# Performance work log

Measured on AMD Instinct MI355X. Metric: run time of the kernel, lower is better.

Reference implementation:

```python
import jax, jax.numpy as jnp
import numpy as np

K = 172   # remainder Hadamard order (had172)
LOG2M = 6 # 2^6 = 64, so hadamard_dim = 172 * 64 = 11008


def _walsh_hadamard_matrix():
    # Dense form of the 6-stage FHT butterfly (Sylvester construction).
    H = np.array([[1.0]], dtype=np.float32)
    for _ in range(LOG2M):
        H = np.block([[H, H], [H, -H]])
    return jnp.asarray(H)  # [64, 64]


def setup_inputs() -> dict:
    key = jax.random.key(0)
    k1, k2 = jax.random.split(key)
    x = jax.random.normal(k1, (2, 4096, 11008), dtype=jnp.float32)
    had_rem_dim = jax.random.normal(k2, (K, K), dtype=jnp.float32) / np.float32(np.sqrt(K))
    return {"x": x, "had_rem_dim": had_rem_dim}


def reference(x, had_rem_dim):
    n = x.shape[-1]                      # 11008 = K * M
    M = n // K                           # 64
    scale = np.float32(1.0 / np.sqrt(n))
    H = _walsh_hadamard_matrix()         # [M, M]
    # view as (..., K, M): FHT over the power-of-two dim, scaled by 1/sqrt(n)
    xr = x.reshape(x.shape[:-1] + (K, M))
    y = jnp.einsum('...km,nm->...kn', xr, H) * scale
    # remainder Hadamard on the K dim: hadK @ input
    y = jnp.einsum('jk,...km->...jm', had_rem_dim, y)
    return y.reshape(x.shape)
```

## Files before the change

kernel.cpp:

```cpp
#include <hip/hip_runtime.h>
#include <hip/hip_bf16.h>

#define KREM 172
#define NDIM 11008
#define JPAD 176
#define KP_HAD 192
#define KP_Y 256

typedef __bf16 bf16x8 __attribute__((ext_vector_type(8)));
typedef float  f32x4  __attribute__((ext_vector_type(4)));
typedef float  f32x2  __attribute__((ext_vector_type(2)));

__global__ void prep_had_kernel(const float* __restrict__ had,
                                __bf16* __restrict__ hadB) {
  int idx = blockIdx.x * 256 + threadIdx.x;
  if (idx >= JPAD * KP_HAD) return;
  int j = idx / KP_HAD;
  int k = idx - j * KP_HAD;
  float v = (j < KREM && k < KREM) ? had[j * KREM + k] * 9.53115434e-3f : 0.0f;
  hadB[idx] = (__bf16)v;
}

__global__ void __launch_bounds__(256, 4) had_fused_kernel(
    const float* __restrict__ x, const __bf16* __restrict__ hadB,
    float* __restrict__ out) {
  __shared__ __bf16 Yt[64 * KP_Y];

  const int tid  = threadIdx.x;
  const int wave = tid >> 6;
  const int lane = tid & 63;
  const size_t rowoff = (size_t)blockIdx.x * NDIM;
  const float* xr   = x + rowoff;
  float*       outr = out + rowoff;

  if (tid < 64) {
    const int e = tid >> 3;
    __bf16* row = Yt + tid * KP_Y;
    const f32x4 z4 = {0.f, 0.f, 0.f, 0.f};
    *(f32x4*)(row + (((22 ^ e) << 3)))     = z4;
    *(f32x4*)(row + (((23 ^ e) << 3)))     = z4;
    *(f32x2*)(row + (((21 ^ e) << 3)) + 4) = (f32x2){0.f, 0.f};
  }

  const int grp = tid >> 3;
  const int lid = tid & 7;

#pragma unroll
  for (int p = 0; p < 6; ++p) {
    const int k = p * 32 + grp;
    if (k < KREM) {
      const float4* seg = (const float4*)(xr + k * 64 + lid * 8);
      float4 a = seg[0], b = seg[1];
      float v[8] = {a.x, a.y, a.z, a.w, b.x, b.y, b.z, b.w};
#pragma unroll
      for (int s = 1; s <= 4; s <<= 1) {
#pragma unroll
        for (int i = 0; i < 8; ++i) {
          if ((i & s) == 0) {
            float u0 = v[i], u1 = v[i + s];
            v[i] = u0 + u1;
            v[i + s] = u0 - u1;
          }
        }
      }
#pragma unroll
      for (int s = 1; s <= 4; s <<= 1) {
        const float sgn = (lid & s) ? -1.0f : 1.0f;
#pragma unroll
        for (int i = 0; i < 8; ++i) {
          float t = __shfl_xor(v[i], s, 64);
          v[i] = __builtin_fmaf(v[i], sgn, t);
        }
      }
      const int kb = k >> 3, ko = k & 7;
      const int kbs = (kb ^ lid) << 3;
#pragma unroll
      for (int i = 0; i < 8; ++i) {
        Yt[(lid * 8 + i) * KP_Y + kbs + ko] = (__bf16)v[i];
      }
    }
  }
  __syncthreads();

  const int l15 = lane & 15;
  const int q   = lane >> 4;
  const int njt = (wave < 3) ? 3 : 2;

#pragma unroll 1
  for (int jl = 0; jl < njt; ++jl) {
    const int jt   = wave + jl * 4;
    const int jrow = jt * 16 + l15;
    const __bf16* hb = hadB + jrow * KP_HAD;
    f32x4 acc[4] = {};
    __builtin_amdgcn_s_setprio(1);
#pragma unroll
    for (int kc = 0; kc < 6; ++kc) {
      const int kbase = kc * 32 + q * 8;
      const bf16x8 bfr = *(const bf16x8*)&hb[kbase];
#pragma unroll
      for (int nt = 0; nt < 4; ++nt) {
        const int n  = nt * 16 + l15;
        const int kb = (kbase >> 3) ^ (n >> 3);
        const bf16x8 afr = *(const bf16x8*)&Yt[n * KP_Y + (kb << 3)];
        acc[nt] = __builtin_amdgcn_mfma_f32_16x16x32_bf16(afr, bfr, acc[nt],
                                                          0, 0, 0);
      }
    }
    __builtin_amdgcn_s_setprio(0);
    if (jrow < KREM) {
#pragma unroll
      for (int nt = 0; nt < 4; ++nt) {
        *(f32x4*)(outr + jrow * 64 + nt * 16 + q * 4) = acc[nt];
      }
    }
  }
}

extern "C" void kernel_launch(void* const* d_in, const int* in_sizes, int n_in,
                              void* d_out, int out_size, void* d_ws, size_t ws_size,
                              hipStream_t stream) {
  const float* x   = (const float*)d_in[0];
  const float* had = (const float*)d_in[1];
  __bf16* hadB = (__bf16*)d_ws;
  float* out = (float*)d_out;
  const int rows = in_sizes[0] / NDIM;

  hipLaunchKernelGGL(prep_had_kernel, dim3((JPAD * KP_HAD + 255) / 256),
                     dim3(256), 0, stream, had, hadB);
  hipLaunchKernelGGL(had_fused_kernel, dim3(rows), dim3(256), 0, stream,
                     x, hadB, out);
}
```

Baseline: 617.6 us.

## Reorder MFMA loop to reuse LDS fragments across j-tiles and use DPP shuffles

The GEMM phase is restructured so the k-chunk loop is outermost. Each wave loads its four Yt A-fragments from LDS once per chunk and reuses them for all of its j-tiles, with 3x4 accumulators held live. This cuts LDS reads about threefold but raises VGPR pressure, which may hurt occupancy under the 4-block launch bound. The xor-1 and xor-2 butterfly shuffles are also replaced with DPP quad_perm moves instead of ds_bpermute-based __shfl_xor.

```diff
diff --git a/kernel.cpp b/kernel.cpp
--- a/kernel.cpp
+++ b/kernel.cpp
@@ -19,6 +19,14 @@
   int k = idx - j * KP_HAD;
   float v = (j < KREM && k < KREM) ? had[j * KREM + k] * 9.53115434e-3f : 0.0f;
   hadB[idx] = (__bf16)v;
+}
+
+__device__ __forceinline__ float dpp_xor(float x, const int ctrl_is_b1) {
+  int s = __builtin_bit_cast(int, x);
+  int t = ctrl_is_b1
+              ? __builtin_amdgcn_update_dpp(0, s, 0xB1, 0xF, 0xF, true)
+              : __builtin_amdgcn_update_dpp(0, s, 0x4E, 0xF, 0xF, true);
+  return __builtin_bit_cast(float, t);
 }
 
 __global__ void __launch_bounds__(256, 4) had_fused_kernel(
@@ -45,6 +53,10 @@
   const int grp = tid >> 3;
   const int lid = tid & 7;
 
+  const float sgn1 = (lid & 1) ? -1.0f : 1.0f;
+  const float sgn2 = (lid & 2) ? -1.0f : 1.0f;
+  const float sgn4 = (lid & 4) ? -1.0f : 1.0f;
+
 #pragma unroll
   for (int p = 0; p < 6; ++p) {
     const int k = p * 32 + grp;
@@ -64,13 +76,19 @@
         }
       }
 #pragma unroll
-      for (int s = 1; s <= 4; s <<= 1) {
-        const float sgn = (lid & s) ? -1.0f : 1.0f;
+      for (int i = 0; i < 8; ++i) {
+        float t = dpp_xor(v[i], 1);
+        v[i] = __builtin_fmaf(v[i], sgn1, t);
+      }
 #pragma unroll
-        for (int i = 0; i < 8; ++i) {
-          float t = __shfl_xor(v[i], s, 64);
-          v[i] = __builtin_fmaf(v[i], sgn, t);
-        }
+      for (int i = 0; i < 8; ++i) {
+        float t = dpp_xor(v[i], 0);
+        v[i] = __builtin_fmaf(v[i], sgn2, t);
+      }
+#pragma unroll
+      for (int i = 0; i < 8; ++i) {
+        float t = __shfl_xor(v[i], 4, 64);
+        v[i] = __builtin_fmaf(v[i], sgn4, t);
       }
       const int kb = k >> 3, ko = k & 7;
       const int kbs = (kb ^ lid) << 3;
@@ -86,31 +104,43 @@
   const int q   = lane >> 4;
   const int njt = (wave < 3) ? 3 : 2;
 
+  f32x4 acc[3][4] = {};
+
+  __builtin_amdgcn_s_setprio(1);
 #pragma unroll 1
-  for (int jl = 0; jl < njt; ++jl) {
-    const int jt   = wave + jl * 4;
-    const int jrow = jt * 16 + l15;
-    const __bf16* hb = hadB + jrow * KP_HAD;
-    f32x4 acc[4] = {};
-    __builtin_amdgcn_s_setprio(1);
+  for (int kc = 0; kc < 6; ++kc) {
+    const int kbase = kc * 32 + q * 8;
+    bf16x8 afr[4];
 #pragma unroll
-    for (int kc = 0; kc < 6; ++kc) {
-      const int kbase = kc * 32 + q * 8;
-      const bf16x8 bfr = *(const bf16x8*)&hb[kbase];
+    for (int nt = 0; nt < 4; ++nt) {
+      const int n  = nt * 16 + l15;
+      const int kb = (kbase >> 3) ^ (n >> 3);
+      afr[nt] = *(const bf16x8*)&Yt[n * KP_Y + (kb << 3)];
+    }
 #pragma unroll
-      for (int nt = 0; nt < 4; ++nt) {
-        const int n  = nt * 16 + l15;
-        const int kb = (kbase >> 3) ^ (n >> 3);
-        const bf16x8 afr = *(const bf16x8*)&Yt[n * KP_Y + (kb << 3)];
-        acc[nt] = __builtin_amdgcn_mfma_f32_16x16x32_bf16(afr, bfr, acc[nt],
-                                                          0, 0, 0);
+    for (int jl = 0; jl < 3; ++jl) {
+      if (jl < njt) {
+        const int jt = wave + jl * 4;
+        const bf16x8 bfr =
+            *(const bf16x8*)&hadB[(jt * 16 + l15) * KP_HAD + kbase];
+#pragma unroll
+        for (int nt = 0; nt < 4; ++nt)
+          acc[jl][nt] = __builtin_amdgcn_mfma_f32_16x16x32_bf16(
+              afr[nt], bfr, acc[jl][nt], 0, 0, 0);
       }
     }
-    __builtin_amdgcn_s_setprio(0);
-    if (jrow < KREM) {
+  }
+  __builtin_amdgcn_s_setprio(0);
+
 #pragma unroll
-      for (int nt = 0; nt < 4; ++nt) {
-        *(f32x4*)(outr + jrow * 64 + nt * 16 + q * 4) = acc[nt];
+  for (int jl = 0; jl < 3; ++jl) {
+    if (jl < njt) {
+      const int j = (wave + jl * 4) * 16 + l15;
+      if (j < KREM) {
+#pragma unroll
+        for (int nt = 0; nt < 4; ++nt) {
+          *(f32x4*)(outr + j * 64 + nt * 16 + q * 4) = acc[jl][nt];
+        }
       }
     }
   }
```

New measurement: 633.7 us. 1.03x slower.
